# Kernel optimization log

Hardware: AMD Instinct MI355X
Metric: run time of the kernel (lower is better)

## Reference

```python
import jax, jax.numpy as jnp
import numpy as np


def setup_inputs() -> dict:
    key = jax.random.key(0)
    ks = jax.random.split(key, 6)
    N, D_IN, H, DH, N_ITEM = 4096, 512, 8, 128, 256
    x = jax.random.normal(ks[0], (N, D_IN), dtype=jnp.float32)
    y = jax.random.normal(ks[1], (N, D_IN), dtype=jnp.float32)
    # linear1/linear2 have NonNeg kernel constraint -> nonnegative weights
    W1 = jax.random.uniform(ks[2], (D_IN, H * DH), dtype=jnp.float32) * 0.05
    W2 = jax.random.uniform(ks[3], (D_IN, H * DH), dtype=jnp.float32) * 0.05
    W3 = jax.random.normal(ks[4], (D_IN, H * DH), dtype=jnp.float32) * 0.05
    # 1x1 conv with 1 output filter over the head axis == weighted sum over heads
    conv_w = jax.random.normal(ks[5], (H,), dtype=jnp.float32)
    return {"x": x, "y": y, "W1": W1, "W2": W2, "W3": W3,
            "conv_w": conv_w, "nItem": N_ITEM}


def reference(x, y, W1, W2, W3, conv_w, nItem):
    N = x.shape[0]
    H = conv_w.shape[0]
    Dh = W1.shape[1] // H
    nSet = N // nItem
    inv_sqrt = 1.0 / jnp.sqrt(jnp.asarray(Dh, dtype=x.dtype))

    q = (x @ W1).reshape(N, H, Dh).transpose(1, 0, 2)   # [H, N, Dh]
    k = (y @ W2).reshape(N, H, Dh).transpose(1, 0, 2)   # [H, N, Dh]
    v = (y @ W3).reshape(N, H, Dh).transpose(1, 0, 2)   # [H, N, Dh]

    # Full cross-set scores, as in the original: [H, N, N]
    scores = jnp.einsum('hnd,hmd->hnm', q, k) * inv_sqrt

    # Block-diagonal y2 matmul == per-set segmented matmul:
    # newx[h, n, s*Dh:(s+1)*Dh] = scores[h, n, s*nItem:(s+1)*nItem] @ v_set_s
    scores_s = scores.reshape(H, N, nSet, nItem)
    v_s = v.reshape(H, nSet, nItem, Dh)
    newx = jnp.einsum('hnsi,hsid->hnsd', scores_s, v_s) / nItem  # [H, N, nSet, Dh]

    # 1x1 conv mixing heads (single output filter, no bias)
    mixed = jnp.einsum('hnsd,h->nsd', newx, conv_w)  # [N, nSet, Dh]

    # isOnlySelf=False branch: reshape [N, nSet*Dh] -> [N, nSet, Dh]
    return mixed
```

## Files before the change

### kernel.cpp

```cpp
#include <hip/hip_runtime.h>
#include <stdint.h>
#include <stddef.h>


typedef short short8 __attribute__((ext_vector_type(8)));
typedef float f32x4 __attribute__((ext_vector_type(4)));

#define AS1 __attribute__((address_space(1)))
#define AS3 __attribute__((address_space(3)))

__device__ __forceinline__ void gl_lds16(const void* g, void* l) {
    __builtin_amdgcn_global_load_lds((AS1 void*)(uintptr_t)g, (AS3 void*)l, 16, 0, 0);
}

__device__ __forceinline__ short f2bf(float f) {
    union { float f; unsigned u; } v; v.f = f;
    unsigned r = v.u + 0x7FFFu + ((v.u >> 16) & 1u);
    return (short)(r >> 16);
}

__global__ __launch_bounds__(256)
void prep(const float* __restrict__ x, const float* __restrict__ y,
          const float* __restrict__ W1, const float* __restrict__ W2,
          const float* __restrict__ W3, short* __restrict__ xb,
          short* __restrict__ yb, short* __restrict__ w1b,
          short* __restrict__ w23t) {
    const int b = blockIdx.x, tid = threadIdx.x;
    if (b < 2048) {
        const float* in = (b < 1024) ? x : y;
        short* o = (b < 1024) ? xb : yb;
        const int i = (b & 1023) * 256 + tid;
        const float4* p = (const float4*)in + (size_t)i * 2;
        float4 a = p[0], c4 = p[1];
        short8 s8;
        s8[0] = f2bf(a.x);  s8[1] = f2bf(a.y);
        s8[2] = f2bf(a.z);  s8[3] = f2bf(a.w);
        s8[4] = f2bf(c4.x); s8[5] = f2bf(c4.y);
        s8[6] = f2bf(c4.z); s8[7] = f2bf(c4.w);
        *((short8*)o + i) = s8;
        return;
    }
    if (b >= 3072) {
        const int i = (b - 3072) * 256 + tid;
        const float4* p = (const float4*)W1 + (size_t)i * 2;
        float4 a = p[0], c4 = p[1];
        short8 s8;
        s8[0] = f2bf(a.x);  s8[1] = f2bf(a.y);
        s8[2] = f2bf(a.z);  s8[3] = f2bf(a.w);
        s8[4] = f2bf(c4.x); s8[5] = f2bf(c4.y);
        s8[6] = f2bf(c4.z); s8[7] = f2bf(c4.w);
        *((short8*)w1b + i) = s8;
        return;
    }
    __shared__ float t[32][33];
    const int b2 = b - 2048;
    const int z = b2 >> 9;
    const float* W = z ? W3 : W2;
    short* Wt = w23t + (size_t)z * 1024 * 512;
    const int b3 = b2 & 511;
    const int bx = (b3 & 31) * 32, by = (b3 >> 5) * 32;
    const int tx = tid & 31, ty = tid >> 5;
    #pragma unroll
    for (int j = 0; j < 4; ++j)
        t[ty + j * 8][tx] = W[(size_t)(by + ty + j * 8) * 1024 + bx + tx];
    __syncthreads();
    #pragma unroll
    for (int j = 0; j < 4; ++j)
        Wt[(size_t)(bx + ty + j * 8) * 512 + by + tx] = f2bf(t[tx][ty + j * 8]);
}

template <int OUTMODE>
__device__ __forceinline__
void gemm_tile(const short* __restrict__ A, int lda,
               const short* __restrict__ Bt, int ldb,
               void* __restrict__ Cout, int ldc, int K,
               int bx, int by, float scale, char* smem) {
    const int tid = threadIdx.x;
    const int wave = tid >> 6, lane = tid & 63;
    const int quad = lane >> 4, ml = lane & 15;
    const int m0 = by * 128, n0 = bx * 128;
    const int wm0 = (wave >> 1) * 64, wn0 = (wave & 1) * 64;
    const int rl = lane >> 3;
    const int ch = lane & 7;
    const int sch = ch ^ rl;

    f32x4 acc[4][4];
    #pragma unroll
    for (int i = 0; i < 4; ++i)
        #pragma unroll
        for (int j = 0; j < 4; ++j) {
            acc[i][j][0] = 0.f; acc[i][j][1] = 0.f;
            acc[i][j][2] = 0.f; acc[i][j][3] = 0.f;
        }

    auto STAGE = [&](char* sbuf, int kt) {
        #pragma unroll
        for (int j = 0; j < 4; ++j) {
            const int r = (wave * 4 + j) * 8 + rl;
            gl_lds16(A + (size_t)(m0 + r) * lda + kt + sch * 8,
                     sbuf + (wave * 4 + j) * 1024 + lane * 16);
        }
        #pragma unroll
        for (int j = 0; j < 4; ++j) {
            const int r = (wave * 4 + j) * 8 + rl;
            gl_lds16(Bt + (size_t)(n0 + r) * ldb + kt + sch * 8,
                     sbuf + 16384 + (wave * 4 + j) * 1024 + lane * 16);
        }
    };

    const int nt = K >> 6;
    STAGE(smem, 0);
    __syncthreads();

    for (int t = 0; t < nt; ++t) {
        char* sbuf = smem + (t & 1) * 32768;
        if (t + 1 < nt)
            STAGE(smem + ((t + 1) & 1) * 32768, (t + 1) * 64);

        const short* sA = (const short*)sbuf;
        const short* sB = (const short*)(sbuf + 16384);
        #pragma unroll
        for (int kk = 0; kk < 2; ++kk) {
            short8 af[4], bfr[4];
            #pragma unroll
            for (int mt = 0; mt < 4; ++mt) {
                const int row = wm0 + mt * 16 + ml;
                af[mt] = *(const short8*)(sA + row * 64 +
                                          (((kk << 2) + quad) ^ (row & 7)) * 8);
            }
            #pragma unroll
            for (int nt2 = 0; nt2 < 4; ++nt2) {
                const int row = wn0 + nt2 * 16 + ml;
                bfr[nt2] = *(const short8*)(sB + row * 64 +
                                            (((kk << 2) + quad) ^ (row & 7)) * 8);
            }
            #pragma unroll
            for (int mt = 0; mt < 4; ++mt)
                #pragma unroll
                for (int nt2 = 0; nt2 < 4; ++nt2)
                    acc[mt][nt2] = __builtin_amdgcn_mfma_f32_16x16x32_bf16(
                        af[mt], bfr[nt2], acc[mt][nt2], 0, 0, 0);
        }
        __syncthreads();
    }

    #pragma unroll
    for (int mt = 0; mt < 4; ++mt)
        #pragma unroll
        for (int nt2 = 0; nt2 < 4; ++nt2) {
            const int col = n0 + wn0 + nt2 * 16 + ml;
            #pragma unroll
            for (int r = 0; r < 4; ++r) {
                const int row = m0 + wm0 + mt * 16 + quad * 4 + r;
                float v = acc[mt][nt2][r];
                if (OUTMODE == 2) v *= scale;
                if (OUTMODE == 0)
                    ((float*)Cout)[(size_t)row * ldc + col] = v;
                else
                    ((short*)Cout)[(size_t)row * ldc + col] = f2bf(v);
            }
        }
}

__device__ __forceinline__ int xcd_swz512(int b) {
    return (b & 7) * 64 + (b >> 3);
}

__global__ __launch_bounds__(256)
void stage_kv(const short* __restrict__ yb, const short* __restrict__ w23t,
              short* __restrict__ kvt) {
    __shared__ char smem[65536];
    const int b = xcd_swz512(blockIdx.x);
    gemm_tile<1>(w23t, 512, yb, 512, kvt, 4096, 512,
                 b & 31, b >> 5, 1.f, smem);
}

__global__ __launch_bounds__(256)
void build_u(const short* __restrict__ kvt, const float* __restrict__ cw,
             short* __restrict__ Ut) {
    __shared__ char smem[65536];
    const int s = blockIdx.x, h = blockIdx.y;
    const float scale = cw[h] * (0.08838834764831845f / 256.0f);
    gemm_tile<2>(kvt + (size_t)(1024 + h * 128) * 4096 + s * 256, 4096,
                 kvt + (size_t)(h * 128) * 4096 + s * 256, 4096,
                 Ut + (size_t)(s * 128) * 1024 + h * 128, 1024, 256,
                 0, 0, scale, smem);
}

__global__ __launch_bounds__(256)
void build_m(const short* __restrict__ Ut, const short* __restrict__ w1b,
             short* __restrict__ M) {
    __shared__ char smem[65536];
    gemm_tile<1>(Ut, 1024, w1b, 1024, M, 512, 1024,
                 blockIdx.x, blockIdx.y, 1.f, smem);
}

__global__ __launch_bounds__(256)
void gemm_out(const short* __restrict__ xb, const short* __restrict__ M,
              float* __restrict__ out) {
    __shared__ char smem[65536];
    const int b = xcd_swz512(blockIdx.x);
    gemm_tile<0>(xb, 512, M, 512, out, 2048, 512,
                 b & 15, b >> 4, 1.f, smem);
}

extern "C" void kernel_launch(void* const* d_in, const int* in_sizes, int n_in,
                              void* d_out, int out_size, void* d_ws, size_t ws_size,
                              hipStream_t stream) {
    const float* x  = (const float*)d_in[0];
    const float* y  = (const float*)d_in[1];
    const float* W1 = (const float*)d_in[2];
    const float* W2 = (const float*)d_in[3];
    const float* W3 = (const float*)d_in[4];
    const float* cw = (const float*)d_in[5];
    float* out = (float*)d_out;

    short* xb   = (short*)d_ws;
    short* yb   = xb   + (size_t)4096 * 512;
    short* w23t = yb   + (size_t)4096 * 512;
    short* w1b  = w23t + (size_t)2048 * 512;
    short* kvt  = w1b  + (size_t)512 * 1024;
    short* Ut   = kvt  + (size_t)2048 * 4096;
    short* M    = Ut   + (size_t)2048 * 1024;

    prep<<<3328, 256, 0, stream>>>(x, y, W1, W2, W3, xb, yb, w1b, w23t);
    stage_kv<<<512, 256, 0, stream>>>(yb, w23t, kvt);
    build_u<<<dim3(16, 8), 256, 0, stream>>>(kvt, cw, Ut);
    build_m<<<dim3(4, 16), 256, 0, stream>>>(Ut, w1b, M);
    gemm_out<<<512, 256, 0, stream>>>(xb, M, out);
}
```

Before: 129.4 us.

## Reassociate output product: compute Q first, drop the M = U·W1 stage

Instead of folding W1 into a small M matrix (U·W1) and multiplying x by it, the code now computes Q = x·W1 alongside the K/V projection in a single combined launch. It then multiplies Q directly by U with K=1024. W1 is now transposed in prep rather than just converted. This removes the low-parallelism build_m kernel and one launch. In exchange it adds more total FLOPs: an extra 4096×1024×512 GEMM, and gemm_out's reduction depth doubles.

```diff
diff --git a/kernel.cpp b/kernel.cpp
--- a/kernel.cpp
+++ b/kernel.cpp
@@ -23,7 +23,7 @@
 void prep(const float* __restrict__ x, const float* __restrict__ y,
           const float* __restrict__ W1, const float* __restrict__ W2,
           const float* __restrict__ W3, short* __restrict__ xb,
-          short* __restrict__ yb, short* __restrict__ w1b,
+          short* __restrict__ yb, short* __restrict__ w1t,
           short* __restrict__ w23t) {
     const int b = blockIdx.x, tid = threadIdx.x;
     if (b < 2048) {
@@ -40,24 +40,17 @@
         *((short8*)o + i) = s8;
         return;
     }
-    if (b >= 3072) {
-        const int i = (b - 3072) * 256 + tid;
-        const float4* p = (const float4*)W1 + (size_t)i * 2;
-        float4 a = p[0], c4 = p[1];
-        short8 s8;
-        s8[0] = f2bf(a.x);  s8[1] = f2bf(a.y);
-        s8[2] = f2bf(a.z);  s8[3] = f2bf(a.w);
-        s8[4] = f2bf(c4.x); s8[5] = f2bf(c4.y);
-        s8[6] = f2bf(c4.z); s8[7] = f2bf(c4.w);
-        *((short8*)w1b + i) = s8;
-        return;
-    }
     __shared__ float t[32][33];
-    const int b2 = b - 2048;
-    const int z = b2 >> 9;
-    const float* W = z ? W3 : W2;
-    short* Wt = w23t + (size_t)z * 1024 * 512;
-    const int b3 = b2 & 511;
+    const float* W; short* Wt; int b3;
+    if (b < 3072) {
+        const int b2 = b - 2048;
+        const int z = b2 >> 9;
+        W = z ? W3 : W2;
+        Wt = w23t + (size_t)z * 1024 * 512;
+        b3 = b2 & 511;
+    } else {
+        W = W1; Wt = w1t; b3 = b - 3072;
+    }
     const int bx = (b3 & 31) * 32, by = (b3 >> 5) * 32;
     const int tx = tid & 31, ty = tid >> 5;
     #pragma unroll
@@ -162,17 +155,20 @@
         }
 }
 
-__device__ __forceinline__ int xcd_swz512(int b) {
-    return (b & 7) * 64 + (b >> 3);
-}
-
-__global__ __launch_bounds__(256)
-void stage_kv(const short* __restrict__ yb, const short* __restrict__ w23t,
-              short* __restrict__ kvt) {
+__global__ __launch_bounds__(256)
+void stage_b(const short* __restrict__ yb, const short* __restrict__ w23t,
+             const short* __restrict__ xb, const short* __restrict__ w1t,
+             short* __restrict__ kvt, short* __restrict__ qb) {
     __shared__ char smem[65536];
-    const int b = xcd_swz512(blockIdx.x);
-    gemm_tile<1>(w23t, 512, yb, 512, kvt, 4096, 512,
-                 b & 31, b >> 5, 1.f, smem);
+    const int b = (blockIdx.x & 7) * 96 + (blockIdx.x >> 3);
+    if (b < 512) {
+        gemm_tile<1>(w23t, 512, yb, 512, kvt, 4096, 512,
+                     b & 31, b >> 5, 1.f, smem);
+    } else {
+        const int b2 = b - 512;
+        gemm_tile<1>(xb, 512, w1t, 512, qb, 1024, 512,
+                     b2 & 7, b2 >> 3, 1.f, smem);
+    }
 }
 
 __global__ __launch_bounds__(256)
@@ -188,19 +184,11 @@
 }
 
 __global__ __launch_bounds__(256)
-void build_m(const short* __restrict__ Ut, const short* __restrict__ w1b,
-             short* __restrict__ M) {
-    __shared__ char smem[65536];
-    gemm_tile<1>(Ut, 1024, w1b, 1024, M, 512, 1024,
-                 blockIdx.x, blockIdx.y, 1.f, smem);
-}
-
-__global__ __launch_bounds__(256)
-void gemm_out(const short* __restrict__ xb, const short* __restrict__ M,
+void gemm_out(const short* __restrict__ qb, const short* __restrict__ Ut,
               float* __restrict__ out) {
     __shared__ char smem[65536];
-    const int b = xcd_swz512(blockIdx.x);
-    gemm_tile<0>(xb, 512, M, 512, out, 2048, 512,
+    const int b = (blockIdx.x & 7) * 64 + (blockIdx.x >> 3);
+    gemm_tile<0>(qb, 1024, Ut, 1024, out, 2048, 1024,
                  b & 15, b >> 4, 1.f, smem);
 }
 
@@ -217,15 +205,14 @@
 
     short* xb   = (short*)d_ws;
     short* yb   = xb   + (size_t)4096 * 512;
-    short* w23t = yb   + (size_t)4096 * 512;
-    short* w1b  = w23t + (size_t)2048 * 512;
-    short* kvt  = w1b  + (size_t)512 * 1024;
-    short* Ut   = kvt  + (size_t)2048 * 4096;
-    short* M    = Ut   + (size_t)2048 * 1024;
-
-    prep<<<3328, 256, 0, stream>>>(x, y, W1, W2, W3, xb, yb, w1b, w23t);
-    stage_kv<<<512, 256, 0, stream>>>(yb, w23t, kvt);
+    short* w1t  = yb   + (size_t)4096 * 512;
+    short* w23t = w1t  + (size_t)1024 * 512;
+    short* kvt  = w23t + (size_t)2048 * 512;
+    short* qb   = kvt  + (size_t)2048 * 4096;
+    short* Ut   = qb   + (size_t)4096 * 1024;
+
+    prep<<<3584, 256, 0, stream>>>(x, y, W1, W2, W3, xb, yb, w1t, w23t);
+    stage_b<<<768, 256, 0, stream>>>(yb, w23t, xb, w1t, kvt, qb);
     build_u<<<dim3(16, 8), 256, 0, stream>>>(kvt, cw, Ut);
-    build_m<<<dim3(4, 16), 256, 0, stream>>>(Ut, w1b, M);
-    gemm_out<<<512, 256, 0, stream>>>(xb, M, out);
-}
+    gemm_out<<<512, 256, 0, stream>>>(qb, Ut, out);
+}
```

Result: slower. 132.2 us (+2.2%).

## Fuse fp32-to-bf16 conversion of x, y, W1 into GEMM staging loads

Applied to the files above, without the earlier changes.

Removes the separate prep passes that converted x, y and W1 to bf16 in workspace. The GEMM tile now loads fp32 directly into registers, converts to bf16, and writes the result to LDS after the MFMA work of the current step, overlapping the next tile's loads with compute. This saves a round trip of intermediate bf16 arrays through global memory. In exchange it doubles the global read bytes for those operands inside the GEMMs, adds register pressure, and gives up the direct global-to-LDS path for those operands.

```diff
diff --git a/kernel.cpp b/kernel.cpp
--- a/kernel.cpp
+++ b/kernel.cpp
@@ -20,44 +20,14 @@
 }
 
 __global__ __launch_bounds__(256)
-void prep(const float* __restrict__ x, const float* __restrict__ y,
-          const float* __restrict__ W1, const float* __restrict__ W2,
-          const float* __restrict__ W3, short* __restrict__ xb,
-          short* __restrict__ yb, short* __restrict__ w1b,
+void prep(const float* __restrict__ W2, const float* __restrict__ W3,
           short* __restrict__ w23t) {
     const int b = blockIdx.x, tid = threadIdx.x;
-    if (b < 2048) {
-        const float* in = (b < 1024) ? x : y;
-        short* o = (b < 1024) ? xb : yb;
-        const int i = (b & 1023) * 256 + tid;
-        const float4* p = (const float4*)in + (size_t)i * 2;
-        float4 a = p[0], c4 = p[1];
-        short8 s8;
-        s8[0] = f2bf(a.x);  s8[1] = f2bf(a.y);
-        s8[2] = f2bf(a.z);  s8[3] = f2bf(a.w);
-        s8[4] = f2bf(c4.x); s8[5] = f2bf(c4.y);
-        s8[6] = f2bf(c4.z); s8[7] = f2bf(c4.w);
-        *((short8*)o + i) = s8;
-        return;
-    }
-    if (b >= 3072) {
-        const int i = (b - 3072) * 256 + tid;
-        const float4* p = (const float4*)W1 + (size_t)i * 2;
-        float4 a = p[0], c4 = p[1];
-        short8 s8;
-        s8[0] = f2bf(a.x);  s8[1] = f2bf(a.y);
-        s8[2] = f2bf(a.z);  s8[3] = f2bf(a.w);
-        s8[4] = f2bf(c4.x); s8[5] = f2bf(c4.y);
-        s8[6] = f2bf(c4.z); s8[7] = f2bf(c4.w);
-        *((short8*)w1b + i) = s8;
-        return;
-    }
     __shared__ float t[32][33];
-    const int b2 = b - 2048;
-    const int z = b2 >> 9;
+    const int z = b >> 9;
     const float* W = z ? W3 : W2;
     short* Wt = w23t + (size_t)z * 1024 * 512;
-    const int b3 = b2 & 511;
+    const int b3 = b & 511;
     const int bx = (b3 & 31) * 32, by = (b3 >> 5) * 32;
     const int tx = tid & 31, ty = tid >> 5;
     #pragma unroll
@@ -69,12 +39,17 @@
         Wt[(size_t)(bx + ty + j * 8) * 512 + by + tx] = f2bf(t[tx][ty + j * 8]);
 }
 
-template <int OUTMODE>
+template <int OUTMODE, bool F32A, bool F32B>
 __device__ __forceinline__
-void gemm_tile(const short* __restrict__ A, int lda,
-               const short* __restrict__ Bt, int ldb,
+void gemm_tile(const void* __restrict__ A_, int lda,
+               const void* __restrict__ Bt_, int ldb,
                void* __restrict__ Cout, int ldc, int K,
                int bx, int by, float scale, char* smem) {
+    const short* A  = (const short*)A_;
+    const float* Af = (const float*)A_;
+    const short* Bt  = (const short*)Bt_;
+    const float* Btf = (const float*)Bt_;
+
     const int tid = threadIdx.x;
     const int wave = tid >> 6, lane = tid & 63;
     const int quad = lane >> 4, ml = lane & 15;
@@ -93,13 +68,15 @@
             acc[i][j][2] = 0.f; acc[i][j][3] = 0.f;
         }
 
-    auto STAGE = [&](char* sbuf, int kt) {
+    auto STAGE_A_LDS = [&](char* sbuf, int kt) {
         #pragma unroll
         for (int j = 0; j < 4; ++j) {
             const int r = (wave * 4 + j) * 8 + rl;
             gl_lds16(A + (size_t)(m0 + r) * lda + kt + sch * 8,
                      sbuf + (wave * 4 + j) * 1024 + lane * 16);
         }
+    };
+    auto STAGE_B_LDS = [&](char* sbuf, int kt) {
         #pragma unroll
         for (int j = 0; j < 4; ++j) {
             const int r = (wave * 4 + j) * 8 + rl;
@@ -107,18 +84,67 @@
                      sbuf + 16384 + (wave * 4 + j) * 1024 + lane * 16);
         }
     };
+    float4 ra[8], rb[8];
+    auto ISSUE_A_F32 = [&](int kt) {
+        #pragma unroll
+        for (int j = 0; j < 4; ++j) {
+            const float* p = Af + (size_t)(m0 + (wave * 4 + j) * 8 + rl) * lda
+                              + kt + sch * 8;
+            ra[j * 2]     = *(const float4*)p;
+            ra[j * 2 + 1] = *(const float4*)(p + 4);
+        }
+    };
+    auto ISSUE_B_F32 = [&](int kt) {
+        #pragma unroll
+        for (int j = 0; j < 4; ++j) {
+            const float* p = Btf + (size_t)(n0 + (wave * 4 + j) * 8 + rl) * ldb
+                               + kt + sch * 8;
+            rb[j * 2]     = *(const float4*)p;
+            rb[j * 2 + 1] = *(const float4*)(p + 4);
+        }
+    };
+    auto WRITE_A_F32 = [&](char* sbuf) {
+        #pragma unroll
+        for (int j = 0; j < 4; ++j) {
+            short8 s;
+            s[0] = f2bf(ra[j*2].x);   s[1] = f2bf(ra[j*2].y);
+            s[2] = f2bf(ra[j*2].z);   s[3] = f2bf(ra[j*2].w);
+            s[4] = f2bf(ra[j*2+1].x); s[5] = f2bf(ra[j*2+1].y);
+            s[6] = f2bf(ra[j*2+1].z); s[7] = f2bf(ra[j*2+1].w);
+            *(short8*)(sbuf + (wave * 4 + j) * 1024 + lane * 16) = s;
+        }
+    };
+    auto WRITE_B_F32 = [&](char* sbuf) {
+        #pragma unroll
+        for (int j = 0; j < 4; ++j) {
+            short8 s;
+            s[0] = f2bf(rb[j*2].x);   s[1] = f2bf(rb[j*2].y);
+            s[2] = f2bf(rb[j*2].z);   s[3] = f2bf(rb[j*2].w);
+            s[4] = f2bf(rb[j*2+1].x); s[5] = f2bf(rb[j*2+1].y);
+            s[6] = f2bf(rb[j*2+1].z); s[7] = f2bf(rb[j*2+1].w);
+            *(short8*)(sbuf + 16384 + (wave * 4 + j) * 1024 + lane * 16) = s;
+        }
+    };
 
     const int nt = K >> 6;
-    STAGE(smem, 0);
+    if constexpr (F32A) { ISSUE_A_F32(0); } else { STAGE_A_LDS(smem, 0); }
+    if constexpr (F32B) { ISSUE_B_F32(0); } else { STAGE_B_LDS(smem, 0); }
+    if constexpr (F32A) WRITE_A_F32(smem);
+    if constexpr (F32B) WRITE_B_F32(smem);
     __syncthreads();
 
     for (int t = 0; t < nt; ++t) {
-        char* sbuf = smem + (t & 1) * 32768;
-        if (t + 1 < nt)
-            STAGE(smem + ((t + 1) & 1) * 32768, (t + 1) * 64);
-
-        const short* sA = (const short*)sbuf;
-        const short* sB = (const short*)(sbuf + 16384);
+        char* cur = smem + (t & 1) * 32768;
+        char* nxt = smem + ((t + 1) & 1) * 32768;
+        if (t + 1 < nt) {
+            if constexpr (F32A) { ISSUE_A_F32((t + 1) * 64); }
+            else                { STAGE_A_LDS(nxt, (t + 1) * 64); }
+            if constexpr (F32B) { ISSUE_B_F32((t + 1) * 64); }
+            else                { STAGE_B_LDS(nxt, (t + 1) * 64); }
+        }
+
+        const short* sA = (const short*)cur;
+        const short* sB = (const short*)(cur + 16384);
         #pragma unroll
         for (int kk = 0; kk < 2; ++kk) {
             short8 af[4], bfr[4];
@@ -140,6 +166,11 @@
                 for (int nt2 = 0; nt2 < 4; ++nt2)
                     acc[mt][nt2] = __builtin_amdgcn_mfma_f32_16x16x32_bf16(
                         af[mt], bfr[nt2], acc[mt][nt2], 0, 0, 0);
+        }
+
+        if (t + 1 < nt) {
+            if constexpr (F32A) WRITE_A_F32(nxt);
+            if constexpr (F32B) WRITE_B_F32(nxt);
         }
         __syncthreads();
     }
@@ -162,17 +193,13 @@
         }
 }
 
-__device__ __forceinline__ int xcd_swz512(int b) {
-    return (b & 7) * 64 + (b >> 3);
-}
-
-__global__ __launch_bounds__(256)
-void stage_kv(const short* __restrict__ yb, const short* __restrict__ w23t,
+__global__ __launch_bounds__(256)
+void stage_kv(const float* __restrict__ y, const short* __restrict__ w23t,
               short* __restrict__ kvt) {
     __shared__ char smem[65536];
-    const int b = xcd_swz512(blockIdx.x);
-    gemm_tile<1>(w23t, 512, yb, 512, kvt, 4096, 512,
-                 b & 31, b >> 5, 1.f, smem);
+    const int b = (blockIdx.x & 7) * 64 + (blockIdx.x >> 3);
+    gemm_tile<1, false, true>(w23t, 512, y, 512, kvt, 4096, 512,
+                              b & 31, b >> 5, 1.f, smem);
 }
 
 __global__ __launch_bounds__(256)
@@ -181,27 +208,28 @@
     __shared__ char smem[65536];
     const int s = blockIdx.x, h = blockIdx.y;
     const float scale = cw[h] * (0.08838834764831845f / 256.0f);
-    gemm_tile<2>(kvt + (size_t)(1024 + h * 128) * 4096 + s * 256, 4096,
-                 kvt + (size_t)(h * 128) * 4096 + s * 256, 4096,
-                 Ut + (size_t)(s * 128) * 1024 + h * 128, 1024, 256,
-                 0, 0, scale, smem);
-}
-
-__global__ __launch_bounds__(256)
-void build_m(const short* __restrict__ Ut, const short* __restrict__ w1b,
+    gemm_tile<2, false, false>(
+        kvt + (size_t)(1024 + h * 128) * 4096 + s * 256, 4096,
+        kvt + (size_t)(h * 128) * 4096 + s * 256, 4096,
+        Ut + (size_t)(s * 128) * 1024 + h * 128, 1024, 256,
+        0, 0, scale, smem);
+}
+
+__global__ __launch_bounds__(256)
+void build_m(const short* __restrict__ Ut, const float* __restrict__ W1,
              short* __restrict__ M) {
     __shared__ char smem[65536];
-    gemm_tile<1>(Ut, 1024, w1b, 1024, M, 512, 1024,
-                 blockIdx.x, blockIdx.y, 1.f, smem);
-}
-
-__global__ __launch_bounds__(256)
-void gemm_out(const short* __restrict__ xb, const short* __restrict__ M,
+    gemm_tile<1, false, true>(Ut, 1024, W1, 1024, M, 512, 1024,
+                              blockIdx.x, blockIdx.y, 1.f, smem);
+}
+
+__global__ __launch_bounds__(256)
+void gemm_out(const float* __restrict__ x, const short* __restrict__ M,
               float* __restrict__ out) {
     __shared__ char smem[65536];
-    const int b = xcd_swz512(blockIdx.x);
-    gemm_tile<0>(xb, 512, M, 512, out, 2048, 512,
-                 b & 15, b >> 4, 1.f, smem);
+    const int b = (blockIdx.x & 7) * 64 + (blockIdx.x >> 3);
+    gemm_tile<0, true, false>(x, 512, M, 512, out, 2048, 512,
+                              b & 15, b >> 4, 1.f, smem);
 }
 
 extern "C" void kernel_launch(void* const* d_in, const int* in_sizes, int n_in,
@@ -215,17 +243,14 @@
     const float* cw = (const float*)d_in[5];
     float* out = (float*)d_out;
 
-    short* xb   = (short*)d_ws;
-    short* yb   = xb   + (size_t)4096 * 512;
-    short* w23t = yb   + (size_t)4096 * 512;
-    short* w1b  = w23t + (size_t)2048 * 512;
-    short* kvt  = w1b  + (size_t)512 * 1024;
+    short* w23t = (short*)d_ws;
+    short* kvt  = w23t + (size_t)2048 * 512;
     short* Ut   = kvt  + (size_t)2048 * 4096;
     short* M    = Ut   + (size_t)2048 * 1024;
 
-    prep<<<3328, 256, 0, stream>>>(x, y, W1, W2, W3, xb, yb, w1b, w23t);
-    stage_kv<<<512, 256, 0, stream>>>(yb, w23t, kvt);
+    prep<<<1024, 256, 0, stream>>>(W2, W3, w23t);
+    stage_kv<<<512, 256, 0, stream>>>(y, w23t, kvt);
     build_u<<<dim3(16, 8), 256, 0, stream>>>(kvt, cw, Ut);
-    build_m<<<dim3(4, 16), 256, 0, stream>>>(Ut, w1b, M);
-    gemm_out<<<512, 256, 0, stream>>>(xb, M, out);
-}
+    build_m<<<dim3(4, 16), 256, 0, stream>>>(Ut, W1, M);
+    gemm_out<<<512, 256, 0, stream>>>(x, M, out);
+}
```

Result: slower. 156.2 us (+20.7%).
